# Kernel tuning notes

Measured on AMD Instinct MI355X. Metric: run time of the kernel, lower is better.

The kernel has to match this reference:

```python
import math
import jax, jax.numpy as jnp
import numpy as np

B, L, D, K = 4, 8192, 256, 2
J = math.ceil(math.log((L - 1) / (K - 1) + 1) / math.log(K))  # 13


def setup_inputs() -> dict:
    key = jax.random.key(0)
    ks = jax.random.split(key, 6)
    h_scale = math.sqrt((math.gamma(K / 2) / math.gamma(J + K / 2)) ** (1.0 / J) / 2)
    return {
        "x": jax.random.normal(ks[0], (B, L, D), dtype=jnp.float32),
        "rms_scale": jnp.ones((D,), dtype=jnp.float32),
        "h0": h_scale * jax.random.normal(ks[1], (D, K), dtype=jnp.float32),
        "h1": h_scale * jax.random.normal(ks[2], (D, K), dtype=jnp.float32),
        "w": (1.0 / math.sqrt(J + 2)) * jax.random.normal(ks[3], (J + 2, D), dtype=jnp.float32),
        "conv_w": jax.random.normal(ks[4], (D, 2 * D), dtype=jnp.float32) / math.sqrt(D),
        "conv_b": jnp.zeros((2 * D,), dtype=jnp.float32),
    }


def _dw_conv(a, h, dilation, d):
    # depthwise dilated 1D conv, VALID padding; a: [B, Lpad, D], h: [1, D, K]
    return jax.lax.conv_general_dilated(
        lhs=a, rhs=h, window_strides=(1,), padding='VALID',
        dimension_numbers=('NLC', 'IOL', 'NLC'),
        rhs_dilation=(dilation,), feature_group_count=d)


def reference(x, rms_scale, h0, h1, w, conv_w, conv_b):
    d = x.shape[-1]
    k = h0.shape[-1]
    n_levels = w.shape[0] - 2
    skip = x
    # RMSNorm (flax default eps=1e-6)
    x = x * jax.lax.rsqrt(jnp.mean(jnp.square(x), axis=-1, keepdims=True) + 1e-6) * rms_scale
    # MultiResLayer (pad_right=False -> left pad, causal)
    h0e = h0[None, :, :]  # [1, D, K]
    h1e = h1[None, :, :]
    y = jnp.zeros_like(x)
    a = x
    for j in range(n_levels):
        dilation = k ** j
        pad = dilation * (k - 1)
        a = jnp.pad(a, ((0, 0), (pad, 0), (0, 0)))
        b = _dw_conv(a, h1e, dilation, d)
        a = _dw_conv(a, h0e, dilation, d)
        y = y + w[j + 1][None, None, :] * b
    y = y + w[None, :1, :] * x + w[None, -1:, :] * a
    # activation -> pointwise conv to 2D -> GLU -> residual
    y = jax.nn.gelu(y)  # approximate=True matches flax nn.gelu default
    y = jnp.einsum('bld,de->ble', y, conv_w) + conv_b
    y = jax.nn.glu(y, axis=-1)
    return y + skip
```

## Files before the change

### kernel.cpp

```cpp
#include <hip/hip_runtime.h>
#include <hip/hip_bf16.h>

#define B_ 4
#define L_ 8192
#define D_ 256
#define J_ 13

typedef __attribute__((ext_vector_type(4))) float f32x4;
typedef __attribute__((ext_vector_type(8))) short bf16x8;
typedef __attribute__((ext_vector_type(8))) unsigned short u16x8;

__device__ __forceinline__ void async_copy16(const void* g, void* l) {
    __builtin_amdgcn_global_load_lds(
        (const __attribute__((address_space(1))) void*)g,
        (__attribute__((address_space(3))) void*)l, 16, 0, 0);
}

__device__ __forceinline__ unsigned int packbf(float a, float b) {
    unsigned int ua = __float_as_uint(a) + 0x8000u;
    unsigned int ub = __float_as_uint(b) + 0x8000u;
    return (ua >> 16) | (ub & 0xFFFF0000u);
}
__device__ __forceinline__ unsigned short packbf1(float a) {
    return (unsigned short)((__float_as_uint(a) + 0x8000u) >> 16);
}

__global__ void rms_wt_kernel(const float* __restrict__ x, const float* __restrict__ scale,
                              ushort* __restrict__ xtb,
                              const float* __restrict__ W, ushort* __restrict__ Wt) {
    __shared__ __align__(16) float sm[32 * 260 + 32];
    int blk = blockIdx.x;
    int tid = threadIdx.x;
    if (blk < 32) {
        float (*tile)[65] = (float(*)[65])sm;
        int dt = blk >> 3, et = blk & 7;
        int d0 = dt * 64, e0 = et * 64;
#pragma unroll
        for (int k = 0; k < 16; ++k) {
            int i = tid + k * 256;
            int r = i >> 6, c = i & 63;
            tile[r][c] = W[(d0 + r) * 512 + e0 + c];
        }
        __syncthreads();
#pragma unroll
        for (int k = 0; k < 16; ++k) {
            int i = tid + k * 256;
            int r = i >> 6, c = i & 63;
            Wt[(e0 + r) * 256 + d0 + c] = packbf1(tile[c][r]);
        }
        return;
    }
    blk -= 32;
    float (*tile)[260] = (float(*)[260])sm;
    float* invl = sm + 32 * 260;
    int b  = blk >> 8;
    int l0 = (blk & 255) << 5;
    const float* src = x + ((size_t)(b * L_ + l0)) * D_;
#pragma unroll
    for (int k = 0; k < 8; ++k) {
        int i = tid + k * 256;
        int r = i >> 6, c4 = i & 63;
        *(float4*)&tile[r][c4 * 4] = *(const float4*)(src + r * D_ + c4 * 4);
    }
    __syncthreads();
    int wave = tid >> 6, lane = tid & 63;
#pragma unroll
    for (int rr = 0; rr < 8; ++rr) {
        int r = wave * 8 + rr;
        float s = 0.f;
#pragma unroll
        for (int q = 0; q < 4; ++q) { float v = tile[r][lane + 64 * q]; s += v * v; }
#pragma unroll
        for (int off = 32; off; off >>= 1) s += __shfl_xor(s, off);
        if (lane == 0) invl[r] = rsqrtf(s * (1.0f / 256.0f) + 1e-6f);
    }
    __syncthreads();
    uint* dst32 = (uint*)xtb;
#pragma unroll
    for (int k = 0; k < 16; ++k) {
        int i = tid + k * 256;
        int d = i >> 4, lp = (i & 15) * 2;
        float v0 = tile[lp][d]     * invl[lp]     * scale[d];
        float v1 = tile[lp + 1][d] * invl[lp + 1] * scale[d];
        dst32[(((size_t)(b * D_ + d)) * L_ + l0 + lp) >> 1] = packbf(v0, v1);
    }
}

#define LEVEL_SMALL(d, jj, buf)                                                  \
    do {                                                                         \
        uint4 pk;                                                                \
        pk.x = packbf(cc[16], cc[17]); pk.y = packbf(cc[18], cc[19]);            \
        pk.z = packbf(cc[20], cc[21]); pk.w = packbf(cc[22], cc[23]);            \
        *(uint4*)((buf) + slot + 16) = pk;                                       \
        pk.x = packbf(cc[24], cc[25]); pk.y = packbf(cc[26], cc[27]);            \
        pk.z = packbf(cc[28], cc[29]); pk.w = packbf(cc[30], cc[31]);            \
        *(uint4*)((buf) + slot + 24) = pk;                                       \
        __syncthreads();                                                         \
        float pt[16];                                                            \
        if (ct > 0) {                                                            \
            uint4 a  = *(const uint4*)((buf) + slot - 40 + 16);                  \
            uint4 bq = *(const uint4*)((buf) + slot - 40 + 24);                  \
            uint uu[8] = {a.x, a.y, a.z, a.w, bq.x, bq.y, bq.z, bq.w};           \
            _Pragma("unroll") for (int q = 0; q < 8; ++q) {                      \
                pt[2*q]   = __uint_as_float(uu[q] << 16);                        \
                pt[2*q+1] = __uint_as_float(uu[q] & 0xFFFF0000u); }              \
        } else { _Pragma("unroll") for (int q = 0; q < 16; ++q) pt[q] = 0.f; }   \
        float wj = w[((jj) + 1) * D_ + c];                                       \
        _Pragma("unroll")                                                        \
        for (int i = 31; i >= 0; --i) {                                          \
            float pv = (i >= (d)) ? cc[i - (d)] : pt[16 + i - (d)];              \
            float nv = h00 * pv + h01 * cc[i];                                   \
            y[i] += wj * (h10 * pv + h11 * cc[i]);                               \
            cc[i] = nv;                                                          \
        }                                                                        \
    } while (0)

__global__ void __launch_bounds__(512) cascade_kernel(
    const ushort* __restrict__ xt, const float* __restrict__ h0,
    const float* __restrict__ h1, const float* __restrict__ w,
    ushort* __restrict__ ygt) {
    __shared__ __align__(16) ushort ex[2 * 512 * 40];
    ushort* bufA = ex;
    ushort* bufB = ex + 512 * 40;
    int blk = blockIdx.x;
    int b = blk >> 7;
    int t = threadIdx.x;
    int ch = t >> 8;
    int ct = t & 255;
    int c = ((blk & 127) << 1) + ch;
    int slot = t * 40;
    float h00 = h0[2*c], h01 = h0[2*c+1];
    float h10 = h1[2*c], h11 = h1[2*c+1];
    float w0 = w[c], wlast = w[14 * D_ + c];

    const ushort* src = xt + ((size_t)(b * D_ + c)) * L_ + ct * 32;
    float cc[32], y[32];
#pragma unroll
    for (int m = 0; m < 4; ++m) {
        u16x8 v = *(const u16x8*)(src + m * 8);
#pragma unroll
        for (int i = 0; i < 8; ++i) cc[m*8+i] = __uint_as_float(((uint)v[i]) << 16);
    }
#pragma unroll
    for (int i = 0; i < 32; ++i) y[i] = w0 * cc[i];

    LEVEL_SMALL(1, 0, bufA);
    LEVEL_SMALL(2, 1, bufB);
    LEVEL_SMALL(4, 2, bufA);
    LEVEL_SMALL(8, 3, bufB);
    LEVEL_SMALL(16, 4, bufA);

#pragma unroll 1
    for (int j = 5; j < J_; ++j) {
        int dT = 1 << (j - 5);
        float wj = w[(j + 1) * D_ + c];
        ushort* buf = (j & 1) ? bufB : bufA;
#pragma unroll
        for (int m = 0; m < 4; ++m) {
            uint4 pk;
            pk.x = packbf(cc[8*m],   cc[8*m+1]); pk.y = packbf(cc[8*m+2], cc[8*m+3]);
            pk.z = packbf(cc[8*m+4], cc[8*m+5]); pk.w = packbf(cc[8*m+6], cc[8*m+7]);
            *(uint4*)(buf + slot + 8 * m) = pk;
        }
        __syncthreads();
        bool has = (ct >= dT);
        int pbase = slot - dT * 40;
#pragma unroll
        for (int h = 0; h < 2; ++h) {
            float pv[16];
            if (has) {
                uint4 a  = *(const uint4*)(buf + pbase + 16 * h);
                uint4 bq = *(const uint4*)(buf + pbase + 16 * h + 8);
                uint uu[8] = {a.x, a.y, a.z, a.w, bq.x, bq.y, bq.z, bq.w};
#pragma unroll
                for (int q = 0; q < 8; ++q) {
                    pv[2*q]   = __uint_as_float(uu[q] << 16);
                    pv[2*q+1] = __uint_as_float(uu[q] & 0xFFFF0000u);
                }
            } else {
#pragma unroll
                for (int q = 0; q < 16; ++q) pv[q] = 0.f;
            }
#pragma unroll
            for (int i = 0; i < 16; ++i) {
                int e = 16 * h + i;
                float nv = h00 * pv[i] + h01 * cc[e];
                y[e] += wj * (h10 * pv[i] + h11 * cc[e]);
                cc[e] = nv;
            }
        }
    }
    ushort* dst = ygt + ((size_t)(b * D_ + c)) * L_ + ct * 32;
#pragma unroll
    for (int m = 0; m < 4; ++m) {
        float g[8];
#pragma unroll
        for (int q = 0; q < 8; ++q) {
            float v = y[8*m+q] + wlast * cc[8*m+q];
            float u = 0.7978845608028654f * (v + 0.044715f * v * v * v);
            g[q] = 0.5f * v * (1.f + tanhf(u));
        }
        uint4 pk;
        pk.x = packbf(g[0], g[1]); pk.y = packbf(g[2], g[3]);
        pk.z = packbf(g[4], g[5]); pk.w = packbf(g[6], g[7]);
        *(uint4*)(dst + 8 * m) = pk;
    }
}

__global__ void trans_kernel(const ushort* __restrict__ ygt, ushort* __restrict__ yg) {
    __shared__ uint tile[64][33];
    int blk = blockIdx.x;
    int b = blk >> 9;
    int rem = blk & 511;
    int dt = rem >> 7, lt = rem & 127;
    int d0 = dt * 64, l0 = lt * 64;
    int tid = threadIdx.x;
    const uint* src = (const uint*)ygt;
#pragma unroll
    for (int k = 0; k < 8; ++k) {
        int i = tid + k * 256;
        int r = i >> 5, cp = i & 31;
        tile[r][cp] = src[(((size_t)(b * D_ + d0 + r)) * L_ + l0) / 2 + cp];
    }
    __syncthreads();
    const ushort* ts = (const ushort*)tile;
#pragma unroll
    for (int k = 0; k < 16; ++k) {
        int i = tid + k * 256;
        int r2 = i >> 6, c2 = i & 63;
        yg[((size_t)(b * L_ + l0 + r2)) * D_ + d0 + c2] = ts[c2 * 66 + r2];
    }
}

__global__ void __launch_bounds__(256) gemm_kernel(
    const ushort* __restrict__ yg, const ushort* __restrict__ Wt,
    const float* __restrict__ cb, const float* __restrict__ x,
    float* __restrict__ out) {
    __shared__ __align__(16) char smem[32768];
    ushort* As = (ushort*)smem;
    ushort* Bs = As + 128 * 64;
    int blk = blockIdx.x;
    int b = blk >> 8;
    int rem = blk & 255;
    int ltile = rem >> 2, et = rem & 3;
    int l0 = ltile * 128, e0 = et * 64;
    int tid = threadIdx.x;
    int wave = tid >> 6, lane = tid & 63;
    int wm = wave >> 1, wn = wave & 1;
    int m0 = wm * 64;

    int srow_in = (lane >> 3);
    int sg = lane & 7;
    int sgg = sg ^ srow_in;
    f32x4 acc[4][4];
#pragma unroll
    for (int i = 0; i < 4; ++i)
#pragma unroll
        for (int j = 0; j < 4; ++j) acc[i][j] = (f32x4)0.f;

    for (int kc = 0; kc < 4; ++kc) {
        __syncthreads();
#pragma unroll
        for (int v = 0; v < 4; ++v) {
            int r = wave * 32 + v * 8 + srow_in;
            async_copy16(yg + ((size_t)(b * L_ + l0 + r)) * D_ + kc * 64 + sgg * 8,
                         As + r * 64 + sg * 8);
            int e = (r < 64) ? (e0 + r) : (256 + e0 + (r - 64));
            async_copy16(Wt + e * 256 + kc * 64 + sgg * 8,
                         Bs + r * 64 + sg * 8);
        }
        __syncthreads();
#pragma unroll
        for (int kk = 0; kk < 2; ++kk) {
            bf16x8 af[4], bfr[4];
            int g = kk * 4 + (lane >> 4);
            int gp = (g ^ (lane & 7)) * 8;
#pragma unroll
            for (int mt = 0; mt < 4; ++mt)
                af[mt] = *(const bf16x8*)(As + (m0 + mt * 16 + (lane & 15)) * 64 + gp);
#pragma unroll
            for (int nt = 0; nt < 4; ++nt) {
                int n = wn * 32 + (nt & 1) * 16 + (nt >> 1) * 64 + (lane & 15);
                bfr[nt] = *(const bf16x8*)(Bs + n * 64 + gp);
            }
#pragma unroll
            for (int mt = 0; mt < 4; ++mt)
#pragma unroll
                for (int nt = 0; nt < 4; ++nt)
                    acc[mt][nt] = __builtin_amdgcn_mfma_f32_16x16x32_bf16(
                        af[mt], bfr[nt], acc[mt][nt], 0, 0, 0);
        }
    }
    __syncthreads();
    float* epi = (float*)smem;
    int row_in = (lane >> 4) * 4;
    int col = lane & 15;
#pragma unroll
    for (int mt = 0; mt < 4; ++mt) {
#pragma unroll
        for (int p = 0; p < 2; ++p) {
            f32x4 uacc = acc[mt][p];
            f32x4 vacc = acc[mt][p + 2];
            int ee = wn * 32 + p * 16 + col;
            float bu = cb[e0 + ee], bv = cb[256 + e0 + ee];
#pragma unroll
            for (int r = 0; r < 4; ++r) {
                int ll = m0 + mt * 16 + row_in + r;
                float u = uacc[r] + bu;
                float v = vacc[r] + bv;
                float g = u / (1.f + __expf(-v));
                epi[ll * 64 + (ee ^ ((ll & 4) ? 16 : 0))] = g;
            }
        }
    }
    __syncthreads();
#pragma unroll
    for (int k = 0; k < 8; ++k) {
        int i = tid + k * 256;
        int ll = i >> 4, e4 = i & 15;
        int exo = (e4 * 4) ^ ((ll & 4) ? 16 : 0);
        float4 gv = *(const float4*)(epi + ll * 64 + exo);
        size_t gidx = ((size_t)(b * L_ + l0 + ll)) * D_ + e0 + e4 * 4;
        float4 xv = *(const float4*)(x + gidx);
        float4 ov;
        ov.x = gv.x + xv.x; ov.y = gv.y + xv.y;
        ov.z = gv.z + xv.z; ov.w = gv.w + xv.w;
        *(float4*)(out + gidx) = ov;
    }
}

extern "C" void kernel_launch(void* const* d_in, const int* in_sizes, int n_in,
                              void* d_out, int out_size, void* d_ws, size_t ws_size,
                              hipStream_t stream) {
    const float* x  = (const float*)d_in[0];
    const float* rs = (const float*)d_in[1];
    const float* h0 = (const float*)d_in[2];
    const float* h1 = (const float*)d_in[3];
    const float* w  = (const float*)d_in[4];
    const float* cw = (const float*)d_in[5];
    const float* cb = (const float*)d_in[6];
    float* out = (float*)d_out;
    char* ws = (char*)d_ws;

    ushort* xtb = (ushort*)ws;
    ushort* ygt = (ushort*)(ws + 16777216);
    ushort* Wt  = (ushort*)(ws + 33554432);
    ushort* yg  = (ushort*)ws;

    rms_wt_kernel<<<1056, 256, 0, stream>>>(x, rs, xtb, cw, Wt);
    cascade_kernel<<<512, 512, 0, stream>>>(xtb, h0, h1, w, ygt);
    trans_kernel<<<2048, 256, 0, stream>>>(ygt, yg);
    gemm_kernel<<<1024, 256, 0, stream>>>(yg, Wt, cb, x, out);
}
```

Baseline: 159.2 us.

## Fuse transpose into GEMM A-tile load and use cheaper GELU/sigmoid math

Removes the separate transpose kernel and has the GEMM read the channel-major cascade output directly. It transposes in registers with byte permutes, writes swizzled LDS, and prefetches the next K chunk into registers. GELU-tanh is rewritten as x*sigmoid(2u) with fast exp and rcp, and the GLU division becomes a reciprocal multiply. This saves a full global round-trip and a kernel launch, at the cost of more register pressure and hand-written waitcnt and barrier scheduling in the GEMM.

```diff
diff --git a/kernel.cpp b/kernel.cpp
--- a/kernel.cpp
+++ b/kernel.cpp
@@ -197,8 +197,8 @@
 #pragma unroll
         for (int q = 0; q < 8; ++q) {
             float v = y[8*m+q] + wlast * cc[8*m+q];
-            float u = 0.7978845608028654f * (v + 0.044715f * v * v * v);
-            g[q] = 0.5f * v * (1.f + tanhf(u));
+            float q2 = 1.5957691216f * v * fmaf(0.044715f, v * v, 1.f);
+            g[q] = v * __builtin_amdgcn_rcpf(1.f + __expf(-q2));
         }
         uint4 pk;
         pk.x = packbf(g[0], g[1]); pk.y = packbf(g[2], g[3]);
@@ -207,33 +207,8 @@
     }
 }
 
-__global__ void trans_kernel(const ushort* __restrict__ ygt, ushort* __restrict__ yg) {
-    __shared__ uint tile[64][33];
-    int blk = blockIdx.x;
-    int b = blk >> 9;
-    int rem = blk & 511;
-    int dt = rem >> 7, lt = rem & 127;
-    int d0 = dt * 64, l0 = lt * 64;
-    int tid = threadIdx.x;
-    const uint* src = (const uint*)ygt;
-#pragma unroll
-    for (int k = 0; k < 8; ++k) {
-        int i = tid + k * 256;
-        int r = i >> 5, cp = i & 31;
-        tile[r][cp] = src[(((size_t)(b * D_ + d0 + r)) * L_ + l0) / 2 + cp];
-    }
-    __syncthreads();
-    const ushort* ts = (const ushort*)tile;
-#pragma unroll
-    for (int k = 0; k < 16; ++k) {
-        int i = tid + k * 256;
-        int r2 = i >> 6, c2 = i & 63;
-        yg[((size_t)(b * L_ + l0 + r2)) * D_ + d0 + c2] = ts[c2 * 66 + r2];
-    }
-}
-
 __global__ void __launch_bounds__(256) gemm_kernel(
-    const ushort* __restrict__ yg, const ushort* __restrict__ Wt,
+    const ushort* __restrict__ ygt, const ushort* __restrict__ Wt,
     const float* __restrict__ cb, const float* __restrict__ x,
     float* __restrict__ out) {
     __shared__ __align__(16) char smem[32768];
@@ -252,32 +227,66 @@
     int srow_in = (lane >> 3);
     int sg = lane & 7;
     int sgg = sg ^ srow_in;
+
+    int lb = tid & 15, db = tid >> 4;
+    const ushort* aPtr = ygt + ((size_t)(b * D_ + db * 4)) * L_ + l0 + lb * 8;
+
     f32x4 acc[4][4];
 #pragma unroll
     for (int i = 0; i < 4; ++i)
 #pragma unroll
         for (int j = 0; j < 4; ++j) acc[i][j] = (f32x4)0.f;
 
+    uint4 ar[4];
+#pragma unroll
+    for (int rr = 0; rr < 4; ++rr) ar[rr] = *(const uint4*)(aPtr + rr * L_);
+
+#pragma unroll
     for (int kc = 0; kc < 4; ++kc) {
         __syncthreads();
 #pragma unroll
         for (int v = 0; v < 4; ++v) {
             int r = wave * 32 + v * 8 + srow_in;
-            async_copy16(yg + ((size_t)(b * L_ + l0 + r)) * D_ + kc * 64 + sgg * 8,
-                         As + r * 64 + sg * 8);
             int e = (r < 64) ? (e0 + r) : (256 + e0 + (r - 64));
             async_copy16(Wt + e * 256 + kc * 64 + sgg * 8,
                          Bs + r * 64 + sg * 8);
         }
-        __syncthreads();
+        __builtin_amdgcn_sched_barrier(0);
+#pragma unroll
+        for (int j = 0; j < 8; ++j) {
+            int q = j >> 1;
+            uint sel = (j & 1) ? 0x07060302u : 0x05040100u;
+            uint w0 = __builtin_amdgcn_perm(((const uint*)&ar[1])[q],
+                                            ((const uint*)&ar[0])[q], sel);
+            uint w1 = __builtin_amdgcn_perm(((const uint*)&ar[3])[q],
+                                            ((const uint*)&ar[2])[q], sel);
+            uint2 wv; wv.x = w0; wv.y = w1;
+            int r = lb * 8 + j;
+            *(uint2*)(As + r * 64 + (((db >> 1) ^ j ^ (lb & 7)) * 8) + (db & 1) * 4) = wv;
+        }
+        if (kc < 3) {
+#pragma unroll
+            for (int rr = 0; rr < 4; ++rr)
+                ar[rr] = *(const uint4*)(aPtr + (size_t)(kc + 1) * 64 * L_ + rr * L_);
+            __builtin_amdgcn_sched_barrier(0);
+            asm volatile("s_waitcnt vmcnt(4) lgkmcnt(0)" ::: "memory");
+        } else {
+            __builtin_amdgcn_sched_barrier(0);
+            asm volatile("s_waitcnt vmcnt(0) lgkmcnt(0)" ::: "memory");
+        }
+        __builtin_amdgcn_s_barrier();
+        __builtin_amdgcn_sched_barrier(0);
 #pragma unroll
         for (int kk = 0; kk < 2; ++kk) {
             bf16x8 af[4], bfr[4];
             int g = kk * 4 + (lane >> 4);
             int gp = (g ^ (lane & 7)) * 8;
 #pragma unroll
-            for (int mt = 0; mt < 4; ++mt)
-                af[mt] = *(const bf16x8*)(As + (m0 + mt * 16 + (lane & 15)) * 64 + gp);
+            for (int mt = 0; mt < 4; ++mt) {
+                int rowA = m0 + mt * 16 + (lane & 15);
+                int gpA = (g ^ (lane & 7) ^ ((rowA >> 3) & 7)) * 8;
+                af[mt] = *(const bf16x8*)(As + rowA * 64 + gpA);
+            }
 #pragma unroll
             for (int nt = 0; nt < 4; ++nt) {
                 int n = wn * 32 + (nt & 1) * 16 + (nt >> 1) * 64 + (lane & 15);
@@ -308,7 +317,7 @@
                 int ll = m0 + mt * 16 + row_in + r;
                 float u = uacc[r] + bu;
                 float v = vacc[r] + bv;
-                float g = u / (1.f + __expf(-v));
+                float g = u * __builtin_amdgcn_rcpf(1.f + __expf(-v));
                 epi[ll * 64 + (ee ^ ((ll & 4) ? 16 : 0))] = g;
             }
         }
@@ -345,10 +354,8 @@
     ushort* xtb = (ushort*)ws;
     ushort* ygt = (ushort*)(ws + 16777216);
     ushort* Wt  = (ushort*)(ws + 33554432);
-    ushort* yg  = (ushort*)ws;
 
     rms_wt_kernel<<<1056, 256, 0, stream>>>(x, rs, xtb, cw, Wt);
     cascade_kernel<<<512, 512, 0, stream>>>(xtb, h0, h1, w, ygt);
-    trans_kernel<<<2048, 256, 0, stream>>>(ygt, yg);
-    gemm_kernel<<<1024, 256, 0, stream>>>(yg, Wt, cb, x, out);
-}
+    gemm_kernel<<<1024, 256, 0, stream>>>(ygt, Wt, cb, x, out);
+}
```

New measurement: 153.0 us. -3.9%, faster.
